# Kernel tuning notes

Hardware: AMD Instinct MI355X
Metric: run time of the kernel (lower is better)

The kernel has to match this reference:

```python
import jax, jax.numpy as jnp
import numpy as np

NEG = -1e30  # stands in for -inf on the diagonal; exp(NEG - max) == 0 exactly


def setup_inputs() -> dict:
    key = jax.random.key(0)
    k1, k2, k3, k4, k5 = jax.random.split(key, 5)
    B, C, H, W = 4, 512, 128, 128
    mid = C // 8  # 64
    x = jax.random.normal(k1, (B, C, H, W), dtype=jnp.float32)
    Wq = jax.random.normal(k2, (mid, C), dtype=jnp.float32) * (1.0 / np.sqrt(C))
    Wk = jax.random.normal(k3, (mid, C), dtype=jnp.float32) * (1.0 / np.sqrt(C))
    Wv = jax.random.normal(k4, (C, C), dtype=jnp.float32) * (1.0 / np.sqrt(C))
    gamma = jax.random.normal(k5, (1,), dtype=jnp.float32) * 0.1
    return {"x": x, "Wq": Wq, "Wk": Wk, "Wv": Wv, "gamma": gamma}


def reference(x, Wq, Wk, Wv, gamma):
    B, C, H, W = x.shape
    # 1x1 convs == channel matmuls
    q = jnp.einsum('bchw,mc->bmhw', x, Wq)  # (B, mid, H, W)
    k = jnp.einsum('bchw,mc->bmhw', x, Wk)
    v = jnp.einsum('bchw,dc->bdhw', x, Wv)  # (B, C, H, W)

    # vertical (H-axis) logits with -inf diagonal: eH[b,i,w,j] = sum_m q[b,m,i,w] k[b,m,j,w]
    eH = jnp.einsum('bmiw,bmjw->biwj', q, k)           # (B, H, W, H)
    diag = jnp.eye(H, dtype=bool)[:, None, :]          # (H, 1, H)
    eH = jnp.where(diag, NEG, eH)

    # horizontal (W-axis) logits: eW[b,h,i,j] = sum_m q[b,m,h,i] k[b,m,h,j]
    eW = jnp.einsum('bmhi,bmhj->bhij', q, k)           # (B, H, W, W)

    # joint softmax over the concatenated H+W logits
    attn = jax.nn.softmax(jnp.concatenate([eH, eW], axis=3), axis=3)  # (B, H, W, H+W)
    aH = attn[:, :, :, :H]  # (B, H, W, H)
    aW = attn[:, :, :, H:]  # (B, H, W, W)

    # attention-weighted value aggregation along each axis
    outH = jnp.einsum('bcjw,biwj->bciw', v, aH)  # (B, C, H, W)
    outW = jnp.einsum('bchj,bhij->bchi', v, aW)  # (B, C, H, W)

    return gamma[0] * (outH + outW) + x
```

## Files before the change

kernel.cpp:

```cpp
#include <hip/hip_runtime.h>
#include <cstdint>
#include <cstddef>

#define NEGV (-1e30f)

constexpr int C_ = 512, H_ = 128, W_ = 128;
constexpr int P_ = 16384;

typedef short bf16x8 __attribute__((ext_vector_type(8)));
typedef float f32x4  __attribute__((ext_vector_type(4)));
#define MFMA16(a, b, c) __builtin_amdgcn_mfma_f32_16x16x32_bf16((a), (b), (c), 0, 0, 0)

#define SWZ128(r, cs) (((r) << 7) + (((((cs) >> 3) ^ ((r) & 7))) << 3) + ((cs) & 7))
#define SWZ64(r, cs)  (((r) << 6) + (((((cs) >> 3) ^ ((r) & 7))) << 3) + ((cs) & 7))

__device__ inline void gl_lds16(const void* g, void* l) {
    __builtin_amdgcn_global_load_lds(
        (const __attribute__((address_space(1))) unsigned int*)g,
        (__attribute__((address_space(3))) unsigned int*)l, 16, 0, 0);
}

__device__ inline unsigned short f2bf(float f) {
    union { float f; uint32_t i; } t; t.f = f;
    uint32_t r = t.i + 0x7FFFu + ((t.i >> 16) & 1u);
    return (unsigned short)(r >> 16);
}

__global__ __launch_bounds__(256) void kwconv(
    const float* __restrict__ Wq, const float* __restrict__ Wk,
    const float* __restrict__ Wv,
    unsigned short* __restrict__ Wqkbf, unsigned short* __restrict__ Wvbf)
{
    const int i4 = (blockIdx.x * 256 + threadIdx.x) * 4;
    const float* src; unsigned short* dst; int off;
    if (i4 < 32768)       { src = Wq + i4;          dst = Wqkbf + i4; }
    else if (i4 < 65536)  { off = i4 - 32768; src = Wk + off; dst = Wqkbf + i4; }
    else                  { off = i4 - 65536; src = Wv + off; dst = Wvbf + off; }
    const float4 v = *(const float4*)src;
    ushort4 u; u.x = f2bf(v.x); u.y = f2bf(v.y); u.z = f2bf(v.z); u.w = f2bf(v.w);
    *(ushort4*)dst = u;
}

__global__ __launch_bounds__(256) void kprep1(
    const float* __restrict__ x, unsigned short* __restrict__ xTbf,
    unsigned short* __restrict__ xbf)
{
    __shared__ float t[32][33];
    const int tid = threadIdx.x;
    const int h0 = (blockIdx.x >> 2) * 32, w0 = (blockIdx.x & 3) * 32;
    const size_t base = (size_t)blockIdx.y * P_;
    {
        const int r = tid >> 3, c4 = (tid & 7) * 4;
        const float4 v = *(const float4*)&x[base + (size_t)(h0 + r) * 128 + w0 + c4];
        t[r][c4] = v.x; t[r][c4 + 1] = v.y; t[r][c4 + 2] = v.z; t[r][c4 + 3] = v.w;
        if (xbf) {
            ushort4 u; u.x = f2bf(v.x); u.y = f2bf(v.y); u.z = f2bf(v.z); u.w = f2bf(v.w);
            *(ushort4*)&xbf[base + (size_t)(h0 + r) * 128 + w0 + c4] = u;
        }
    }
    __syncthreads();
    {
        const int wr = tid >> 3, hc = (tid & 7) * 4;
        ushort4 u;
        u.x = f2bf(t[hc][wr]);     u.y = f2bf(t[hc + 1][wr]);
        u.z = f2bf(t[hc + 2][wr]); u.w = f2bf(t[hc + 3][wr]);
        *(ushort4*)&xTbf[base + (size_t)(w0 + wr) * 128 + h0 + hc] = u;
    }
}

__global__ __launch_bounds__(256) void kprep2(
    const float* __restrict__ x, const unsigned short* __restrict__ xbf,
    unsigned short* __restrict__ xbfT)
{
    __shared__ float tf[32][33];
    __shared__ unsigned short tb[32][34];
    const int tid = threadIdx.x;
    const int p0 = blockIdx.x * 32, c0 = blockIdx.y * 32, b = blockIdx.z;
    const int r = tid >> 3, c4 = (tid & 7) * 4;
    if (xbf) {
        const ushort4 v = *(const ushort4*)&xbf[((size_t)(b * C_ + c0 + r)) * P_ + p0 + c4];
        tb[r][c4] = v.x; tb[r][c4 + 1] = v.y; tb[r][c4 + 2] = v.z; tb[r][c4 + 3] = v.w;
        __syncthreads();
        const int pr = tid >> 3, cc = (tid & 7) * 4;
        ushort4 u;
        u.x = tb[cc][pr];     u.y = tb[cc + 1][pr];
        u.z = tb[cc + 2][pr]; u.w = tb[cc + 3][pr];
        *(ushort4*)&xbfT[((size_t)b * P_ + p0 + pr) * C_ + c0 + cc] = u;
    } else {
        const float4 v = *(const float4*)&x[((size_t)(b * C_ + c0 + r)) * P_ + p0 + c4];
        tf[r][c4] = v.x; tf[r][c4 + 1] = v.y; tf[r][c4 + 2] = v.z; tf[r][c4 + 3] = v.w;
        __syncthreads();
        const int pr = tid >> 3, cc = (tid & 7) * 4;
        ushort4 u;
        u.x = f2bf(tf[cc][pr]);     u.y = f2bf(tf[cc + 1][pr]);
        u.z = f2bf(tf[cc + 2][pr]); u.w = f2bf(tf[cc + 3][pr]);
        *(ushort4*)&xbfT[((size_t)b * P_ + p0 + pr) * C_ + c0 + cc] = u;
    }
}

__global__ __launch_bounds__(256) void kgemmqk(
    const unsigned short* __restrict__ A, const unsigned short* __restrict__ Bm,
    unsigned short* __restrict__ outbf)
{
    __shared__ __attribute__((aligned(16))) unsigned short sA[2][128 * 64];
    __shared__ __attribute__((aligned(16))) unsigned short sB[2][128 * 64];
    const int tid = threadIdx.x;
    const int pbase = blockIdx.x * 128, b = blockIdx.z;
    const int lane = tid & 63, wv = tid >> 6;
    const int m0 = (wv >> 1) * 64, p0 = (wv & 1) * 64;
    const int fr = lane & 15, fq = lane >> 4;

    f32x4 acc[4][4];
#pragma unroll
    for (int i = 0; i < 4; i++)
#pragma unroll
        for (int j = 0; j < 4; j++) acc[i][j] = (f32x4){0.f, 0.f, 0.f, 0.f};

    const size_t brow0 = ((size_t)b * P_ + pbase) * 512;

#define QK_STAGE(chunk, buf) {                                                  \
        const int kc_ = (chunk) * 64;                                           \
        _Pragma("unroll")                                                       \
        for (int rep = 0; rep < 4; rep++) {                                     \
            const int idx = rep * 256 + tid;                                    \
            const int r_ = idx >> 3, kgs = (idx & 7) ^ (r_ & 7);                \
            gl_lds16(&A[(size_t)r_ * 512 + kc_ + kgs * 8], &sA[buf][idx * 8]);  \
            gl_lds16(&Bm[brow0 + (size_t)r_ * 512 + kc_ + kgs * 8], &sB[buf][idx * 8]); \
        } }

    QK_STAGE(0, 0);
    int cur = 0;
    for (int chunk = 0; chunk < 8; ++chunk) {
        if (chunk < 7) {
            QK_STAGE(chunk + 1, cur ^ 1);
            asm volatile("s_waitcnt vmcnt(8)" ::: "memory");
        } else {
            asm volatile("s_waitcnt vmcnt(0)" ::: "memory");
        }
        __builtin_amdgcn_s_barrier();
#pragma unroll
        for (int kk = 0; kk < 64; kk += 32) {
            bf16x8 af[4], bfv[4];
#pragma unroll
            for (int t = 0; t < 4; t++) af[t]  = *(const bf16x8*)&sA[cur][SWZ64(m0 + t * 16 + fr, kk + fq * 8)];
#pragma unroll
            for (int t = 0; t < 4; t++) bfv[t] = *(const bf16x8*)&sB[cur][SWZ64(p0 + t * 16 + fr, kk + fq * 8)];
#pragma unroll
            for (int i = 0; i < 4; i++)
#pragma unroll
                for (int j = 0; j < 4; j++)
                    acc[i][j] = MFMA16(af[i], bfv[j], acc[i][j]);
        }
        if (chunk < 7) __builtin_amdgcn_s_barrier();
        cur ^= 1;
    }
#undef QK_STAGE

#pragma unroll
    for (int tj = 0; tj < 4; tj++) {
        const int p_g = pbase + p0 + tj * 16 + fr;
        const size_t rowo = ((size_t)b * P_ + p_g) * 128;
#pragma unroll
        for (int ti = 0; ti < 4; ti++) {
            const int mk = m0 + ti * 16 + fq * 4;
            ushort4 u;
            u.x = f2bf(acc[ti][tj][0]); u.y = f2bf(acc[ti][tj][1]);
            u.z = f2bf(acc[ti][tj][2]); u.w = f2bf(acc[ti][tj][3]);
            *(ushort4*)&outbf[rowo + mk] = u;
        }
    }
}

__global__ __launch_bounds__(256) void klogitsP(
    const unsigned short* __restrict__ qkP,
    unsigned short* __restrict__ PR, unsigned short* __restrict__ PC,
    float* __restrict__ MR, float* __restrict__ SR,
    float* __restrict__ MC, float* __restrict__ SC)
{
    __shared__ __attribute__((aligned(16))) unsigned short sPM[128 * 136];
    __shared__ float red[2][128];
    const int tid = threadIdx.x;
    const int s = blockIdx.x, b = blockIdx.y, mode = blockIdx.z;
    const int rowMul  = mode ? 1 : 128;
    const int rowStep = mode ? 128 : 1;
    unsigned short* PP = mode ? PC : PR;
    float* Ma = mode ? MC : MR;
    float* Sa = mode ? SC : SR;
    const size_t qbase = (size_t)b * P_ * 128;
    const int rb = s * rowMul;
#pragma unroll
    for (int rep = 0; rep < 8; rep++) {
        const int idx = rep * 256 + tid;
        const int mkg = idx & 15, i = idx >> 4;
        *(uint4*)&sPM[i * 136 + mkg * 8] =
            *(const uint4*)&qkP[qbase + (size_t)(rb + i * rowStep) * 128 + mkg * 8];
    }
    __syncthreads();

    const int lane = tid & 63, wv = tid >> 6;
    const int i0 = (wv >> 1) * 64, j0 = (wv & 1) * 64;
    const int fr = lane & 15, fq = lane >> 4;
    const int jh = wv & 1;

    f32x4 acc[4][4];
#pragma unroll
    for (int i = 0; i < 4; i++)
#pragma unroll
        for (int j = 0; j < 4; j++) acc[i][j] = (f32x4){0.f, 0.f, 0.f, 0.f};

#pragma unroll
    for (int kk = 0; kk < 64; kk += 32) {
        bf16x8 af[4], bfv[4];
#pragma unroll
        for (int t = 0; t < 4; t++) af[t]  = *(const bf16x8*)&sPM[(i0 + t * 16 + fr) * 136 + kk + fq * 8];
#pragma unroll
        for (int t = 0; t < 4; t++) bfv[t] = *(const bf16x8*)&sPM[(j0 + t * 16 + fr) * 136 + 64 + kk + fq * 8];
#pragma unroll
        for (int i = 0; i < 4; i++)
#pragma unroll
            for (int j = 0; j < 4; j++)
                acc[i][j] = MFMA16(af[i], bfv[j], acc[i][j]);
    }

    float mrow[4][4];
#pragma unroll
    for (int ti = 0; ti < 4; ti++)
#pragma unroll
        for (int r = 0; r < 4; r++) {
            const int i_g = i0 + ti * 16 + fq * 4 + r;
            float mx = -3.0e38f;
#pragma unroll
            for (int tj = 0; tj < 4; tj++) {
                const int j_g = j0 + tj * 16 + fr;
                float v = acc[ti][tj][r];
                if (mode && i_g == j_g) v = NEGV;
                mx = fmaxf(mx, v);
            }
#pragma unroll
            for (int off = 8; off > 0; off >>= 1) mx = fmaxf(mx, __shfl_xor(mx, off));
            red[jh][i_g] = mx;
        }
    __syncthreads();
#pragma unroll
    for (int ti = 0; ti < 4; ti++)
#pragma unroll
        for (int r = 0; r < 4; r++) {
            const int i_g = i0 + ti * 16 + fq * 4 + r;
            mrow[ti][r] = fmaxf(red[0][i_g], red[1][i_g]);
        }

    float wsum[4][4];
    unsigned short* Pb = PP + ((size_t)(b * 128 + s)) * P_;
#pragma unroll
    for (int ti = 0; ti < 4; ti++)
#pragma unroll
        for (int r = 0; r < 4; r++) {
            const int i_g = i0 + ti * 16 + fq * 4 + r;
            const float m_ = mrow[ti][r];
            float ts = 0.f;
#pragma unroll
            for (int tj = 0; tj < 4; tj++) {
                const int j_g = j0 + tj * 16 + fr;
                float v = acc[ti][tj][r];
                if (mode && i_g == j_g) v = NEGV;
                const float e = __expf(v - m_);
                ts += e;
                Pb[(size_t)i_g * 128 + j_g] = f2bf(e);
            }
#pragma unroll
            for (int off = 8; off > 0; off >>= 1) ts += __shfl_xor(ts, off);
            wsum[ti][r] = ts;
        }
    __syncthreads();
#pragma unroll
    for (int ti = 0; ti < 4; ti++)
#pragma unroll
        for (int r = 0; r < 4; r++)
            red[jh][i0 + ti * 16 + fq * 4 + r] = wsum[ti][r];
    __syncthreads();
    if (fr == 0 && jh == 0) {
#pragma unroll
        for (int ti = 0; ti < 4; ti++)
#pragma unroll
            for (int r = 0; r < 4; r++) {
                const int i_g = i0 + ti * 16 + fq * 4 + r;
                const size_t o = (((size_t)b * 128 + s) << 7) + i_g;
                Ma[o] = mrow[ti][r];
                Sa[o] = red[0][i_g] + red[1][i_g];
            }
    }
}

__global__ __launch_bounds__(256) void kcomb(
    const float* __restrict__ MR, const float* __restrict__ SR,
    const float* __restrict__ MC, const float* __restrict__ SC,
    float* __restrict__ FR, float* __restrict__ FC)
{
    const int idx = blockIdx.x * 256 + threadIdx.x;
    const int b = idx >> 14, rem = idx & 16383;
    const int h = rem >> 7, w = rem & 127;
    const int ro = (b << 14) + (h << 7) + w;
    const int co = (b << 14) + (w << 7) + h;
    const float mR = MR[ro], sR = SR[ro];
    const float mC = MC[co], sC = SC[co];
    const float m = fmaxf(mR, mC);
    const float eR = __expf(mR - m), eC = __expf(mC - m);
    const float inv = 1.0f / (sR * eR + sC * eC);
    FR[ro] = eR * inv;
    FC[co] = eC * inv;
}

__global__ __launch_bounds__(256) void kagg2(
    const unsigned short* __restrict__ PR, const unsigned short* __restrict__ PC,
    const float* __restrict__ x, const unsigned short* __restrict__ xbf,
    const unsigned short* __restrict__ xTbf,
    const float* __restrict__ FR, const float* __restrict__ FC,
    unsigned short* __restrict__ ySumR, unsigned short* __restrict__ ySumC)
{
    __shared__ __attribute__((aligned(16))) unsigned short sAttn[128 * 128];
    __shared__ __attribute__((aligned(16))) unsigned short sX[128 * 128];
    __shared__ float sF[128];
    const int tid = threadIdx.x;
    const int s = blockIdx.x, b = blockIdx.y, mode = blockIdx.z;
    const int lane = tid & 63, wv = tid >> 6;
    const int m0 = (wv >> 1) * 64, n0 = (wv & 1) * 64;
    const int fr = lane & 15, fq = lane >> 4;

    const unsigned short* At = (mode ? PC : PR) + ((size_t)(b * 128 + s)) * P_;
#pragma unroll
    for (int rep = 0; rep < 8; rep++) {
        const int idx = rep * 256 + tid;
        const int r = idx >> 4, sl = idx & 15;
        gl_lds16(&At[(size_t)r * 128 + (sl ^ (r & 7)) * 8], &sAttn[idx * 8]);
    }
    const float* Fsel = mode ? FC : FR;
    if (tid < 128) sF[tid] = Fsel[(((size_t)b * 128 + s) << 7) + tid];

    unsigned short* yS = mode ? ySumC : ySumR;
    const unsigned short* Xsrc = mode ? xTbf : xbf;

    for (int ct = 0; ct < 4; ct++) {
        if (Xsrc) {
            const unsigned short* Xs = &Xsrc[((size_t)(b * C_ + ct * 128)) * P_ + s * 128];
#pragma unroll
            for (int rep = 0; rep < 8; rep++) {
                const int idx = rep * 256 + tid;
                const int r = idx >> 4, sl = idx & 15;
                gl_lds16(&Xs[(size_t)r * P_ + (sl ^ (r & 7)) * 8], &sX[idx * 8]);
            }
        } else {
            const float* Xf = &x[((size_t)(b * C_ + ct * 128)) * P_ + s * 128];
#pragma unroll
            for (int rep = 0; rep < 16; rep++) {
                const int idx = rep * 256 + tid;
                const int jq = idx & 31, cc = idx >> 5;
                const float4 v = *(const float4*)&Xf[(size_t)cc * P_ + jq * 4];
                ushort4 u; u.x = f2bf(v.x); u.y = f2bf(v.y); u.z = f2bf(v.z); u.w = f2bf(v.w);
                *(ushort4*)&sX[SWZ128(cc, jq * 4)] = u;
            }
        }
        __syncthreads();

        f32x4 acc[4][4];
#pragma unroll
        for (int i = 0; i < 4; i++)
#pragma unroll
            for (int j = 0; j < 4; j++) acc[i][j] = (f32x4){0.f, 0.f, 0.f, 0.f};

#pragma unroll
        for (int kk = 0; kk < 128; kk += 32) {
            bf16x8 af[4], bfv[4];
#pragma unroll
            for (int t = 0; t < 4; t++) {
                const int rc = m0 + t * 16 + fr;
                af[t] = *(const bf16x8*)&sX[SWZ128(rc, kk + fq * 8)];
            }
#pragma unroll
            for (int t = 0; t < 4; t++) {
                const int ri = n0 + t * 16 + fr;
                bfv[t] = *(const bf16x8*)&sAttn[SWZ128(ri, kk + fq * 8)];
            }
#pragma unroll
            for (int i = 0; i < 4; i++)
#pragma unroll
                for (int j = 0; j < 4; j++)
                    acc[i][j] = MFMA16(af[i], bfv[j], acc[i][j]);
        }

        const int cg0 = ct * 128 + m0 + fq * 4;
#pragma unroll
        for (int tj = 0; tj < 4; tj++) {
            const int i_g = n0 + tj * 16 + fr;
            const float fsc = sF[i_g];
            const size_t p = mode ? ((size_t)i_g * 128 + s) : ((size_t)s * 128 + i_g);
            unsigned short* rowp = yS + ((size_t)b * P_ + p) * 512;
#pragma unroll
            for (int ti = 0; ti < 4; ti++) {
                ushort4 u;
                u.x = f2bf(acc[ti][tj][0] * fsc); u.y = f2bf(acc[ti][tj][1] * fsc);
                u.z = f2bf(acc[ti][tj][2] * fsc); u.w = f2bf(acc[ti][tj][3] * fsc);
                *(ushort4*)&rowp[cg0 + ti * 16] = u;
            }
        }
        __syncthreads();
    }
}

__global__ __launch_bounds__(512, 2) void kfinal256(
    const unsigned short* __restrict__ Wvbf,
    const unsigned short* __restrict__ yR,
    const unsigned short* __restrict__ yC,
    float* __restrict__ outf,
    const float* __restrict__ addx,
    const float* __restrict__ gammap)
{
    __shared__ __attribute__((aligned(16))) unsigned short sM[2][256 * 64];
    __shared__ __attribute__((aligned(16))) unsigned short sP[2][256 * 64];
    const int tid = threadIdx.x;
    const int pbase = blockIdx.x * 256, mt = blockIdx.y, b = blockIdx.z;
    const int lane = tid & 63, wv = tid >> 6;
    const int m0w = (wv >> 2) * 128;
    const int p0w = (wv & 3) * 64;
    const int fr = lane & 15, fq = lane >> 4;

    f32x4 acc[4][8];
#pragma unroll
    for (int i = 0; i < 4; i++)
#pragma unroll
        for (int j = 0; j < 8; j++) acc[i][j] = (f32x4){0.f, 0.f, 0.f, 0.f};

    const unsigned short* Arow = Wvbf + (size_t)(mt * 256) * 512;
    const size_t brow = ((size_t)b * P_ + pbase) * 512;

#define FIN_STAGE(chunk, buf) {                                                 \
        const int kc_ = ((chunk) & 7) * 64;                                     \
        const unsigned short* Bp = ((chunk) < 8 ? yR : yC) + brow + kc_;        \
        const unsigned short* Ap = Arow + kc_;                                  \
        _Pragma("unroll")                                                       \
        for (int rep = 0; rep < 4; rep++) {                                     \
            const int idx = rep * 512 + tid;                                    \
            const int r_ = idx >> 3, kgs = (idx & 7) ^ (r_ & 7);                \
            gl_lds16(&Ap[(size_t)r_ * 512 + kgs * 8], &sM[buf][idx * 8]);       \
            gl_lds16(&Bp[(size_t)r_ * 512 + kgs * 8], &sP[buf][idx * 8]);       \
        } }

    FIN_STAGE(0, 0);
    int cur = 0;
    for (int chunk = 0; chunk < 16; ++chunk) {
        if (chunk < 15) {
            FIN_STAGE(chunk + 1, cur ^ 1);
            asm volatile("s_waitcnt vmcnt(8)" ::: "memory");
        } else {
            asm volatile("s_waitcnt vmcnt(0)" ::: "memory");
        }
        __builtin_amdgcn_s_barrier();
#pragma unroll
        for (int kk = 0; kk < 64; kk += 32) {
            bf16x8 bp[4], am[8];
#pragma unroll
            for (int t = 0; t < 4; t++) bp[t] = *(const bf16x8*)&sP[cur][SWZ64(p0w + t * 16 + fr, kk + fq * 8)];
#pragma unroll
            for (int t = 0; t < 8; t++) am[t] = *(const bf16x8*)&sM[cur][SWZ64(m0w + t * 16 + fr, kk + fq * 8)];
            __builtin_amdgcn_s_setprio(1);
#pragma unroll
            for (int i = 0; i < 4; i++)
#pragma unroll
                for (int j = 0; j < 8; j++)
                    acc[i][j] = MFMA16(bp[i], am[j], acc[i][j]);
            __builtin_amdgcn_s_setprio(0);
        }
        if (chunk < 15) __builtin_amdgcn_s_barrier();
        cur ^= 1;
    }
#undef FIN_STAGE

    const float g = gammap[0];
#pragma unroll
    for (int ti = 0; ti < 4; ti++) {
        const int p_g = pbase + p0w + ti * 16 + fq * 4;
#pragma unroll
        for (int tj = 0; tj < 8; tj++) {
            const int m_g = mt * 256 + m0w + tj * 16 + fr;
            const size_t off = ((size_t)(b * 512 + m_g)) * P_ + p_g;
            const float4 xa = *(const float4*)&addx[off];
            float4 o;
            o.x = fmaf(g, acc[ti][tj][0], xa.x);
            o.y = fmaf(g, acc[ti][tj][1], xa.y);
            o.z = fmaf(g, acc[ti][tj][2], xa.z);
            o.w = fmaf(g, acc[ti][tj][3], xa.w);
            *(float4*)&outf[off] = o;
        }
    }
}

extern "C" void kernel_launch(void* const* d_in, const int* in_sizes, int n_in,
                              void* d_out, int out_size, void* d_ws, size_t ws_size,
                              hipStream_t stream) {
    const float* x     = (const float*)d_in[0];
    const float* Wq    = (const float*)d_in[1];
    const float* Wk    = (const float*)d_in[2];
    const float* Wv    = (const float*)d_in[3];
    const float* gamma = (const float*)d_in[4];
    float* out = (float*)d_out;

    char* base = (char*)d_ws;
    unsigned short* Wqkbf = (unsigned short*)base;             base += 131072;
    unsigned short* Wvbf  = (unsigned short*)base;             base += 524288;
    unsigned short* xTbf  = (unsigned short*)base;             base += 67108864;
    unsigned short* xbfT  = (unsigned short*)base;             base += 67108864;
    unsigned short* qkP   = (unsigned short*)base;             base += 16777216;
    char*           freeRC = base;                             base += 67108864;
    unsigned short* PR    = (unsigned short*)base;             base += 16777216;
    unsigned short* PC    = (unsigned short*)base;             base += 16777216;
    unsigned short* ySumR = (unsigned short*)base;             base += 67108864;
    float*          MR    = (float*)base;                      base += 262144;
    float*          SR    = (float*)base;                      base += 262144;
    float*          MC    = (float*)base;                      base += 262144;
    float*          SC    = (float*)base;                      base += 262144;
    float*          FR    = (float*)base;                      base += 262144;
    float*          FC    = (float*)base;                      base += 262144;
    unsigned short* ySumC = (unsigned short*)freeRC;
    const size_t used = (size_t)(base - (char*)d_ws);
    unsigned short* xbf = nullptr;
    if (ws_size >= used + 67108864) { xbf = (unsigned short*)base; base += 67108864; }

    kwconv<<<320, 256, 0, stream>>>(Wq, Wk, Wv, Wqkbf, Wvbf);
    kprep1<<<dim3(16, 2048), 256, 0, stream>>>(x, xTbf, xbf);
    kprep2<<<dim3(512, 16, 4), 256, 0, stream>>>(x, xbf, xbfT);
    kgemmqk<<<dim3(128, 1, 4), 256, 0, stream>>>(Wqkbf, xbfT, qkP);
    klogitsP<<<dim3(128, 4, 2), 256, 0, stream>>>(qkP, PR, PC, MR, SR, MC, SC);
    kcomb<<<256, 256, 0, stream>>>(MR, SR, MC, SC, FR, FC);
    kagg2<<<dim3(128, 4, 2), 256, 0, stream>>>(PR, PC, x, xbf, xTbf, FR, FC, ySumR, ySumC);
    kfinal256<<<dim3(64, 2, 4), 512, 0, stream>>>(Wvbf, ySumR, ySumC, out, x, gamma);
}
```

Baseline: 524.6 us.

## Pre-sum row and column aggregates before final value GEMM and swizzle block order

Adds a separate elementwise kernel that sums the row and column aggregated activations (bf16) into one buffer. The final GEMM then contracts over 512 channels instead of two concatenated 512 halves, halving its MFMA work and B-operand reads. It also flattens the grid and remaps block indices so neighbouring blocks are spread across batch, position and channel tiles. The cost is an extra pass that reads two 64 MB buffers and writes one, plus an extra bf16 rounding of the sum.

```diff
diff --git a/kernel.cpp b/kernel.cpp
--- a/kernel.cpp
+++ b/kernel.cpp
@@ -24,6 +24,17 @@
     union { float f; uint32_t i; } t; t.f = f;
     uint32_t r = t.i + 0x7FFFu + ((t.i >> 16) & 1u);
     return (unsigned short)(r >> 16);
+}
+__device__ inline uint32_t bfadd2(uint32_t a, uint32_t b) {
+    union { uint32_t i; float f; } alo, ahi, blo, bhi;
+    alo.i = a << 16; ahi.i = a & 0xffff0000u;
+    blo.i = b << 16; bhi.i = b & 0xffff0000u;
+    const float lo = alo.f + blo.f, hi = ahi.f + bhi.f;
+    return (uint32_t)f2bf(lo) | ((uint32_t)f2bf(hi) << 16);
+}
+__device__ inline uint4 bfadd8(const uint4 a, const uint4 b) {
+    uint4 r; r.x = bfadd2(a.x, b.x); r.y = bfadd2(a.y, b.y);
+    r.z = bfadd2(a.z, b.z); r.w = bfadd2(a.w, b.w); return r;
 }
 
 __global__ __launch_bounds__(256) void kwconv(
@@ -406,10 +417,19 @@
     }
 }
 
+__global__ __launch_bounds__(256) void kadd(
+    const unsigned short* __restrict__ a, const unsigned short* __restrict__ b,
+    unsigned short* __restrict__ o)
+{
+    const size_t n4 = (size_t)4 * P_ * 512 / 8;
+    for (size_t i = (size_t)blockIdx.x * 256 + threadIdx.x; i < n4;
+         i += (size_t)gridDim.x * 256)
+        ((uint4*)o)[i] = bfadd8(((const uint4*)a)[i], ((const uint4*)b)[i]);
+}
+
 __global__ __launch_bounds__(512, 2) void kfinal256(
     const unsigned short* __restrict__ Wvbf,
-    const unsigned short* __restrict__ yR,
-    const unsigned short* __restrict__ yC,
+    const unsigned short* __restrict__ yS,
     float* __restrict__ outf,
     const float* __restrict__ addx,
     const float* __restrict__ gammap)
@@ -417,7 +437,10 @@
     __shared__ __attribute__((aligned(16))) unsigned short sM[2][256 * 64];
     __shared__ __attribute__((aligned(16))) unsigned short sP[2][256 * 64];
     const int tid = threadIdx.x;
-    const int pbase = blockIdx.x * 256, mt = blockIdx.y, b = blockIdx.z;
+    const int swz = (blockIdx.x & 7) * 64 + (blockIdx.x >> 3);
+    const int mt = swz & 1;
+    const int pbase = ((swz >> 1) & 63) * 256;
+    const int b = swz >> 7;
     const int lane = tid & 63, wv = tid >> 6;
     const int m0w = (wv >> 2) * 128;
     const int p0w = (wv & 3) * 64;
@@ -433,8 +456,8 @@
     const size_t brow = ((size_t)b * P_ + pbase) * 512;
 
 #define FIN_STAGE(chunk, buf) {                                                 \
-        const int kc_ = ((chunk) & 7) * 64;                                     \
-        const unsigned short* Bp = ((chunk) < 8 ? yR : yC) + brow + kc_;        \
+        const int kc_ = (chunk) * 64;                                           \
+        const unsigned short* Bp = yS + brow + kc_;                             \
         const unsigned short* Ap = Arow + kc_;                                  \
         _Pragma("unroll")                                                       \
         for (int rep = 0; rep < 4; rep++) {                                     \
@@ -446,8 +469,8 @@
 
     FIN_STAGE(0, 0);
     int cur = 0;
-    for (int chunk = 0; chunk < 16; ++chunk) {
-        if (chunk < 15) {
+    for (int chunk = 0; chunk < 8; ++chunk) {
+        if (chunk < 7) {
             FIN_STAGE(chunk + 1, cur ^ 1);
             asm volatile("s_waitcnt vmcnt(8)" ::: "memory");
         } else {
@@ -469,7 +492,7 @@
                     acc[i][j] = MFMA16(bp[i], am[j], acc[i][j]);
             __builtin_amdgcn_s_setprio(0);
         }
-        if (chunk < 15) __builtin_amdgcn_s_barrier();
+        if (chunk < 7) __builtin_amdgcn_s_barrier();
         cur ^= 1;
     }
 #undef FIN_STAGE
@@ -520,6 +543,7 @@
     float*          FR    = (float*)base;                      base += 262144;
     float*          FC    = (float*)base;                      base += 262144;
     unsigned short* ySumC = (unsigned short*)freeRC;
+    unsigned short* ySumS = xbfT;
     const size_t used = (size_t)(base - (char*)d_ws);
     unsigned short* xbf = nullptr;
     if (ws_size >= used + 67108864) { xbf = (unsigned short*)base; base += 67108864; }
@@ -531,5 +555,6 @@
     klogitsP<<<dim3(128, 4, 2), 256, 0, stream>>>(qkP, PR, PC, MR, SR, MC, SC);
     kcomb<<<256, 256, 0, stream>>>(MR, SR, MC, SC, FR, FC);
     kagg2<<<dim3(128, 4, 2), 256, 0, stream>>>(PR, PC, x, xbf, xTbf, FR, FC, ySumR, ySumC);
-    kfinal256<<<dim3(64, 2, 4), 512, 0, stream>>>(Wvbf, ySumR, ySumC, out, x, gamma);
-}
+    kadd<<<2048, 256, 0, stream>>>(ySumR, ySumC, ySumS);
+    kfinal256<<<512, 512, 0, stream>>>(Wvbf, ySumS, out, x, gamma);
+}
```

After: 532.1 us. Within noise of the previous version (+1.4%).
